# Kernel tuning notes

Hardware: AMD Instinct MI355X
Metric: run time of the kernel (lower is better)

Reference implementation:

```python
import jax, jax.numpy as jnp
import numpy as np

HEAD_DIM = 64
N_HEADS = 12
ROPE_BASE = 10000.0


def _rope_tables(seq_len, head_dim, dtype=jnp.float32):
    half = head_dim // 2
    inv_freq = 1.0 / (ROPE_BASE ** (jnp.arange(0, half, dtype=jnp.float32) / half))
    pos = jnp.arange(seq_len, dtype=jnp.float32)
    freqs = pos[:, None] * inv_freq[None, :]  # (s, half)
    return jnp.cos(freqs).astype(dtype), jnp.sin(freqs).astype(dtype)


def _apply_rope(t, cos, sin):
    # t: (b, h, s, d); rotate-half convention on full head_dim (rope_fraction=1.0)
    d = t.shape[-1]
    t1, t2 = t[..., : d // 2], t[..., d // 2 :]
    cos = cos[None, None, :, :]
    sin = sin[None, None, :, :]
    return jnp.concatenate([t1 * cos - t2 * sin, t1 * sin + t2 * cos], axis=-1)


def setup_inputs() -> dict:
    key = jax.random.key(0)
    ks = jax.random.split(key, 6)
    b, s, d_model = 16, 512, 768
    x = jax.random.normal(ks[0], (b, s, d_model), dtype=jnp.float32)
    chain_ids = jax.random.randint(ks[1], (b, s), 0, 2, dtype=jnp.int32)
    attention_mask = jnp.ones((b, s), dtype=bool)
    inner = N_HEADS * HEAD_DIM
    scale = 0.02
    Wq = jax.random.normal(ks[2], (d_model, inner), dtype=jnp.float32) * scale
    Wk = jax.random.normal(ks[3], (d_model, inner), dtype=jnp.float32) * scale
    Wv = jax.random.normal(ks[4], (d_model, inner), dtype=jnp.float32) * scale
    Wo = jax.random.normal(ks[5], (inner, d_model), dtype=jnp.float32) * scale
    return {"x": x, "chain_ids": chain_ids, "attention_mask": attention_mask,
            "Wq": Wq, "Wk": Wk, "Wv": Wv, "Wo": Wo}


def reference(x, chain_ids, attention_mask, Wq, Wk, Wv, Wo):
    b, s, _ = x.shape
    h, d = N_HEADS, HEAD_DIM
    scale = d ** (-0.5)

    def proj(W):
        return jnp.einsum('bse,ef->bsf', x, W).reshape(b, s, h, d).transpose(0, 2, 1, 3)

    q = proj(Wq)  # (b, h, s, d)
    k = proj(Wk)
    v = proj(Wv)

    cos, sin = _rope_tables(s, d, x.dtype)
    q_rope = _apply_rope(q, cos, sin)
    k_rope = _apply_rope(k, cos, sin)

    scores_intra = jnp.einsum('bhsd,bhtd->bhst', q_rope, k_rope) * scale
    scores_inter = jnp.einsum('bhsd,bhtd->bhst', q, k) * scale

    # intra-chain mask (b, 1, s, s)
    intra = (chain_ids[:, None, :, None] == chain_ids[:, None, None, :])
    merged = jnp.where(intra, scores_intra, scores_inter)

    # additive padding mask (b, 1, 1, s)
    pad = jnp.where(attention_mask[:, None, None, :], 0.0, -jnp.inf).astype(x.dtype)
    merged = merged + pad

    attn = jax.nn.softmax(merged, axis=-1)
    attn = jnp.nan_to_num(attn, nan=0.0)

    out = jnp.einsum('bhst,bhtd->bhsd', attn, v)
    out = out.transpose(0, 2, 1, 3).reshape(b, s, h * d)
    return jnp.einsum('bsf,fe->bse', out, Wo)
```

## Files before the change

kernel.cpp:

```cpp
#include <hip/hip_runtime.h>
#include <stdint.h>
#include <math.h>

#define NB 16
#define NS 512
#define NH 12
#define ND 64
#define NE 768
#define NF 768

typedef __attribute__((ext_vector_type(4))) float  f32x4;
typedef __attribute__((ext_vector_type(8))) short  bf16x8;

#define AS1(p) ((const __attribute__((address_space(1))) unsigned int*)(p))
#define AS3(p) ((__attribute__((address_space(3))) unsigned int*)(p))

__device__ __forceinline__ short f2bf(float f) {
    unsigned u = __builtin_bit_cast(unsigned, f);
    u += 0x7FFFu + ((u >> 16) & 1u);
    return (short)(u >> 16);
}
__device__ __forceinline__ float bf2f(short s) {
    unsigned u = ((unsigned)(unsigned short)s) << 16;
    return __builtin_bit_cast(float, u);
}
__device__ __forceinline__ unsigned pkbf2(float a, float b) {
    return (unsigned)(unsigned short)f2bf(a) | ((unsigned)(unsigned short)f2bf(b) << 16);
}

#define MFMA16(a, b, c) __builtin_amdgcn_mfma_f32_16x16x32_bf16((a), (b), (c), 0, 0, 0)

__device__ __forceinline__ bf16x8 lds_rd8(const short* base, int row, int cb) {
    return *(const bf16x8*)((const char*)base + (((row) * 128 + (cb)) ^ (((row) & 7) << 4)));
}

__global__ __launch_bounds__(256) void prep_all_kernel(
    const float* __restrict__ x, short* __restrict__ xb,
    const float* __restrict__ Wq, const float* __restrict__ Wk,
    const float* __restrict__ Wv, const float* __restrict__ Wo,
    short* __restrict__ Wqt, short* __restrict__ Wkt,
    short* __restrict__ Wvt, short* __restrict__ Wot,
    float* __restrict__ cos_t, float* __restrict__ sin_t,
    const unsigned char* __restrict__ m, int* __restrict__ flag) {
    const int bid = blockIdx.x;
    if (bid < 64) {
        int i = bid * 256 + threadIdx.x;
        int p = i >> 5, j = i & 31;
        float inv_freq = powf(10000.0f, -(float)j / 32.0f);
        float ang = (float)p * inv_freq;
        cos_t[i] = cosf(ang);
        sin_t[i] = sinf(ang);
        return;
    }
    if (bid == 64) {
        __shared__ int any;
        if (threadIdx.x == 0) any = 0;
        __syncthreads();
        int acc = 0;
        for (int i = threadIdx.x; i < NB * NS; i += 256)
            if ((i & 3) && m[i]) acc = 1;
        if (acc) atomicOr(&any, 1);
        __syncthreads();
        if (threadIdx.x == 0) *flag = any;
        return;
    }
    if (bid < 641) {
        int idx = bid - 65;
        int zz = idx / 144, r2 = idx % 144;
        const float* W  = (zz == 0) ? Wq  : (zz == 1) ? Wk  : (zz == 2) ? Wv  : Wo;
        short*       Wt = (zz == 0) ? Wqt : (zz == 1) ? Wkt : (zz == 2) ? Wvt : Wot;
        const int k0 = (r2 / 12) * 64, n0 = (r2 % 12) * 64;
        __shared__ float t[64][65];
        for (int u = threadIdx.x; u < 4096; u += 256) {
            int r = u >> 6, c = u & 63;
            t[r][c] = W[(size_t)(k0 + r) * 768 + n0 + c];
        }
        __syncthreads();
        for (int u = threadIdx.x; u < 4096; u += 256) {
            int c = u >> 6, r = u & 63;
            Wt[(size_t)(n0 + c) * 768 + k0 + r] = f2bf(t[r][c]);
        }
        return;
    }
    int i = ((bid - 641) * 256 + threadIdx.x) * 8;
    float4 a = *(const float4*)&x[i];
    float4 b = *(const float4*)&x[i + 4];
    bf16x8 r = { f2bf(a.x), f2bf(a.y), f2bf(a.z), f2bf(a.w),
                 f2bf(b.x), f2bf(b.y), f2bf(b.z), f2bf(b.w) };
    *(bf16x8*)&xb[i] = r;
}

__global__ __launch_bounds__(256) void gemm_qkv_kernel(const short* __restrict__ xb,
    const short* __restrict__ Wqt, const short* __restrict__ Wkt, const short* __restrict__ Wvt,
    const float* __restrict__ cos_t, const float* __restrict__ sin_t,
    short* __restrict__ qo, short* __restrict__ ko, short* __restrict__ kpo,
    short* __restrict__ vto) {
    const int id = blockIdx.x;
    const int xcd = id & 7, rest = id >> 3;
    const int mq = rest / 18;
    const int nz = rest % 18;
    const int z  = nz / 6;
    const int n0 = (nz % 6) * 128;
    const int m0 = (xcd * 8 + mq) * 128;
    const short* Bt = (z == 0) ? Wqt : (z == 1) ? Wkt : Wvt;
    short*       O  = (z == 0) ? qo  : (z == 1) ? ko  : vto;
    __shared__ short As[2][128 * 64], Bs[2][128 * 64];
    const int tid = threadIdx.x, lane = tid & 63, wave = tid >> 6;
    const int g = lane >> 4, l15 = lane & 15;
    const int wm = wave >> 1, wn = wave & 1;
    f32x4 acc[4][4];
    #pragma unroll
    for (int i = 0; i < 4; ++i)
        #pragma unroll
        for (int j = 0; j < 4; ++j) acc[i][j] = (f32x4){0.f, 0.f, 0.f, 0.f};

    auto STAGE = [&](short* Ad, short* Bd, int kt) {
        const char* Asrc = (const char*)(xb + (size_t)m0 * 768 + kt * 64);
        const char* Bsrc = (const char*)(Bt + (size_t)n0 * 768 + kt * 64);
        #pragma unroll
        for (int p = 0; p < 4; ++p) {
            int dstoff = (wave * 4 + p) * 1024;
            int off = dstoff + lane * 16;
            int row = off >> 7, slot = off & 127;
            int srcs = slot ^ ((row & 7) << 4);
            __builtin_amdgcn_global_load_lds(AS1(Asrc + (size_t)row * 1536 + srcs),
                                             AS3((char*)Ad + dstoff), 16, 0, 0);
            __builtin_amdgcn_global_load_lds(AS1(Bsrc + (size_t)row * 1536 + srcs),
                                             AS3((char*)Bd + dstoff), 16, 0, 0);
        }
    };
    auto COMPUTE = [&](const short* Asb, const short* Bsb) {
        __builtin_amdgcn_s_setprio(1);
        #pragma unroll
        for (int h2 = 0; h2 < 2; ++h2) {
            bf16x8 af[4], bfr[4];
            const int cb = h2 * 64 + g * 16;
            #pragma unroll
            for (int i = 0; i < 4; ++i) {
                af[i]  = lds_rd8(Asb, wm * 64 + i * 16 + l15, cb);
                bfr[i] = lds_rd8(Bsb, wn * 64 + i * 16 + l15, cb);
            }
            #pragma unroll
            for (int i = 0; i < 4; ++i)
                #pragma unroll
                for (int j = 0; j < 4; ++j)
                    acc[i][j] = MFMA16(af[i], bfr[j], acc[i][j]);
        }
        __builtin_amdgcn_s_setprio(0);
    };

    STAGE(As[0], Bs[0], 0);
    asm volatile("s_waitcnt vmcnt(0)" ::: "memory");
    __builtin_amdgcn_s_barrier();
    int cur = 0;
    for (int kt = 0; kt < 11; ++kt) {
        STAGE(As[cur ^ 1], Bs[cur ^ 1], kt + 1);
        COMPUTE(As[cur], Bs[cur]);
        asm volatile("s_waitcnt vmcnt(0)" ::: "memory");
        __builtin_amdgcn_s_barrier();
        cur ^= 1;
    }
    COMPUTE(As[cur], Bs[cur]);

    const int hh = (n0 + wn * 64) >> 6;
    #pragma unroll
    for (int i = 0; i < 4; ++i)
        #pragma unroll
        for (int r = 0; r < 4; ++r) {
            int mm = m0 + wm * 64 + i * 16 + g * 4 + r;
            int bb = mm >> 9, ss = mm & 511;
            if (z == 2) {
                #pragma unroll
                for (int j = 0; j < 4; ++j) {
                    int dd = j * 16 + l15;
                    O[(((size_t)bb * NH + hh) * ND + dd) * NS + ss] = f2bf(acc[i][j][r]);
                }
            } else {
                size_t base = (((size_t)bb * NH + hh) * NS + ss) * ND;
                #pragma unroll
                for (int j = 0; j < 4; ++j)
                    O[base + j * 16 + l15] = f2bf(acc[i][j][r]);
                if (z == 1) {
                    #pragma unroll
                    for (int p2 = 0; p2 < 2; ++p2) {
                        int jf = p2 * 16 + l15;
                        float c = cos_t[ss * 32 + jf], s = sin_t[ss * 32 + jf];
                        float t1 = acc[i][p2][r], t2 = acc[i][p2 + 2][r];
                        kpo[base + jf]      = f2bf(t1 * c - t2 * s);
                        kpo[base + 32 + jf] = f2bf(t1 * s + t2 * c);
                    }
                }
            }
        }
}

__global__ __launch_bounds__(256) void attn_fused_kernel(
    const short* __restrict__ qr, const short* __restrict__ kr, const short* __restrict__ kp,
    const short* __restrict__ vt,
    const float* __restrict__ cos_t, const float* __restrict__ sin_t,
    const int* __restrict__ chain, const void* __restrict__ amask,
    const int* __restrict__ mflag, short* __restrict__ aout) {
    const int lid = blockIdx.x;
    const int xcd = lid & 7, idx = lid >> 3;
    const int qt = idx & 7, bhl = idx >> 3;
    const int bh = xcd * 24 + bhl;
    const int b = bh / 12, h = bh - (bh / 12) * 12;
    const int q0 = qt * 64;

    __shared__ short Kr_s[4096];
    __shared__ short Kp_s[4096];
    __shared__ short Vt_s[4096];
    __shared__ short P_s[4096];
    __shared__ int   ck_a[512];
    __shared__ float kb_a[512];

    const int tid = threadIdx.x, lane = tid & 63, wave = tid >> 6;
    const int g = lane >> 4, l15 = lane & 15;
    const int m_u8 = *mflag;
    const size_t bhNS = (size_t)bh * NS;
    const float SC = 0.18033688011f;

    for (int u = tid; u < NS; u += 256) {
        int gidx = b * NS + u;
        ck_a[u] = chain[gidx];
        int ok = m_u8 ? (int)((const unsigned char*)amask)[gidx] : ((const int*)amask)[gidx];
        kb_a[u] = ok ? 0.f : -INFINITY;
    }
    const char* qrsC = (const char*)(qr + (bhNS + q0) * ND);
    #pragma unroll
    for (int p = 0; p < 2; ++p) {
        int dstoff = (wave * 2 + p) * 1024;
        int off = dstoff + lane * 16;
        int row = off >> 7, slot = off & 127;
        int srcs = slot ^ ((row & 7) << 4);
        __builtin_amdgcn_global_load_lds(AS1(qrsC + (size_t)row * 128 + srcs),
                                         AS3((char*)Kr_s + dstoff), 16, 0, 0);
    }
    __syncthreads();
    const int qrow = wave * 16 + l15;
    bf16x8 fqr0 = lds_rd8(Kr_s, qrow, g * 16);
    bf16x8 fqr1 = lds_rd8(Kr_s, qrow, 64 + g * 16);
    bf16x8 fqp0, fqp1;
    {
        int pos = q0 + qrow;
        float4 c0 = *(const float4*)&cos_t[pos * 32 + g * 8];
        float4 c1 = *(const float4*)&cos_t[pos * 32 + g * 8 + 4];
        float4 s0 = *(const float4*)&sin_t[pos * 32 + g * 8];
        float4 s1 = *(const float4*)&sin_t[pos * 32 + g * 8 + 4];
        float cc[8] = {c0.x, c0.y, c0.z, c0.w, c1.x, c1.y, c1.z, c1.w};
        float ss[8] = {s0.x, s0.y, s0.z, s0.w, s1.x, s1.y, s1.z, s1.w};
        #pragma unroll
        for (int j = 0; j < 8; ++j) {
            float t1 = bf2f(fqr0[j]), t2 = bf2f(fqr1[j]);
            fqp0[j] = f2bf(t1 * cc[j] - t2 * ss[j]);
            fqp1[j] = f2bf(t1 * ss[j] + t2 * cc[j]);
        }
    }
    const int cqv = ck_a[q0 + qrow];

    float m_run = -INFINITY, l_run = 0.f;
    f32x4 accO[4];
    #pragma unroll
    for (int t = 0; t < 4; ++t) accO[t] = (f32x4){0.f, 0.f, 0.f, 0.f};

    const char* krC = (const char*)(kr + bhNS * ND);
    const char* kpC = (const char*)(kp + bhNS * ND);
    const char* vtC = (const char*)(vt + bhNS * ND);

    for (int kv = 0; kv < 8; ++kv) {
        const int k0s = kv * 64;
        __syncthreads();
        #pragma unroll
        for (int p = 0; p < 2; ++p) {
            int dstoff = (wave * 2 + p) * 1024;
            int off = dstoff + lane * 16;
            int row = off >> 7, slot = off & 127;
            int srcs = slot ^ ((row & 7) << 4);
            size_t koff = (size_t)(k0s + row) * 128 + srcs;
            __builtin_amdgcn_global_load_lds(AS1(krC + koff), AS3((char*)Kr_s + dstoff), 16, 0, 0);
            __builtin_amdgcn_global_load_lds(AS1(kpC + koff), AS3((char*)Kp_s + dstoff), 16, 0, 0);
            __builtin_amdgcn_global_load_lds(AS1(vtC + (size_t)row * 1024 + k0s * 2 + srcs),
                                             AS3((char*)Vt_s + dstoff), 16, 0, 0);
        }
        __syncthreads();

        float pm[4][4];
        float tm = -INFINITY;
        __builtin_amdgcn_s_setprio(1);
        #pragma unroll
        for (int t = 0; t < 4; ++t) {
            bf16x8 akr0 = lds_rd8(Kr_s, t * 16 + l15, g * 16);
            bf16x8 akr1 = lds_rd8(Kr_s, t * 16 + l15, 64 + g * 16);
            bf16x8 akp0 = lds_rd8(Kp_s, t * 16 + l15, g * 16);
            bf16x8 akp1 = lds_rd8(Kp_s, t * 16 + l15, 64 + g * 16);
            f32x4 sr = (f32x4){0.f, 0.f, 0.f, 0.f};
            f32x4 sp = (f32x4){0.f, 0.f, 0.f, 0.f};
            sr = MFMA16(akr0, fqr0, sr);
            sr = MFMA16(akr1, fqr1, sr);
            sp = MFMA16(akp0, fqp0, sp);
            sp = MFMA16(akp1, fqp1, sp);
            int4   ck4 = *(const int4*)&ck_a[k0s + t * 16 + g * 4];
            float4 kb4 = *(const float4*)&kb_a[k0s + t * 16 + g * 4];
            const int   ckk[4] = {ck4.x, ck4.y, ck4.z, ck4.w};
            const float kbb[4] = {kb4.x, kb4.y, kb4.z, kb4.w};
            #pragma unroll
            for (int r = 0; r < 4; ++r) {
                float sv = (cqv == ckk[r]) ? sp[r] : sr[r];
                sv = sv * SC + kbb[r];
                pm[t][r] = sv;
                tm = fmaxf(tm, sv);
            }
        }
        __builtin_amdgcn_s_setprio(0);

        tm = fmaxf(tm, __shfl_xor(tm, 16));
        tm = fmaxf(tm, __shfl_xor(tm, 32));
        bool skip = __all(tm - m_run <= 8.f);
        float mnew, fac;
        if (skip) { mnew = m_run; fac = 1.f; }
        else      { mnew = fmaxf(m_run, tm); fac = exp2f(m_run - mnew); }
        float psum = 0.f;
        if (mnew == -INFINITY) {
            #pragma unroll
            for (int t = 0; t < 4; ++t)
                #pragma unroll
                for (int r = 0; r < 4; ++r) pm[t][r] = 0.f;
            fac = 1.f;
        } else {
            #pragma unroll
            for (int t = 0; t < 4; ++t)
                #pragma unroll
                for (int r = 0; r < 4; ++r) {
                    float p = exp2f(pm[t][r] - mnew);
                    pm[t][r] = p;
                    psum += p;
                }
        }
        psum += __shfl_xor(psum, 16);
        psum += __shfl_xor(psum, 32);
        l_run = l_run * fac + psum;
        m_run = mnew;

        char* pwave = (char*)P_s + wave * 2048;
        int psw = (l15 & 7) << 4;
        #pragma unroll
        for (int t = 0; t < 4; ++t) {
            unsigned u0 = pkbf2(pm[t][0], pm[t][1]);
            unsigned u1 = pkbf2(pm[t][2], pm[t][3]);
            uint2 pk = {u0, u1};
            *(uint2*)(pwave + ((l15 * 128 + t * 32 + g * 8) ^ psw)) = pk;
        }
        if (!skip) {
            float f4[4];
            #pragma unroll
            for (int r = 0; r < 4; ++r) f4[r] = __shfl(fac, g * 4 + r);
            #pragma unroll
            for (int t = 0; t < 4; ++t) {
                f32x4 a = accO[t];
                a[0] *= f4[0]; a[1] *= f4[1]; a[2] *= f4[2]; a[3] *= f4[3];
                accO[t] = a;
            }
        }
        bf16x8 pa0 = *(const bf16x8*)(pwave + ((l15 * 128 + g * 16) ^ psw));
        bf16x8 pa1 = *(const bf16x8*)(pwave + ((l15 * 128 + 64 + g * 16) ^ psw));
        __builtin_amdgcn_s_setprio(1);
        #pragma unroll
        for (int dt = 0; dt < 4; ++dt) {
            bf16x8 vb0 = lds_rd8(Vt_s, dt * 16 + l15, g * 16);
            bf16x8 vb1 = lds_rd8(Vt_s, dt * 16 + l15, 64 + g * 16);
            accO[dt] = MFMA16(pa0, vb0, accO[dt]);
            accO[dt] = MFMA16(pa1, vb1, accO[dt]);
        }
        __builtin_amdgcn_s_setprio(0);
    }

    float inv[4];
    #pragma unroll
    for (int r = 0; r < 4; ++r) {
        float lv = __shfl(l_run, g * 4 + r);
        inv[r] = (lv > 0.f) ? 1.f / lv : 0.f;
    }
    #pragma unroll
    for (int dt = 0; dt < 4; ++dt)
        #pragma unroll
        for (int r = 0; r < 4; ++r) {
            int row = b * NS + q0 + wave * 16 + g * 4 + r;
            aout[(size_t)row * NF + h * ND + dt * 16 + l15] = f2bf(accO[dt][r] * inv[r]);
        }
}

__global__ __launch_bounds__(256) void gemm_out_kernel(const short* __restrict__ A,
    const short* __restrict__ Wot, float* __restrict__ out) {
    const int id = blockIdx.x;
    const int xcd = id & 7, rest = id >> 3;
    const int mq = rest / 6;
    const int n0 = (rest % 6) * 128;
    const int m0 = (xcd * 16 + mq) * 64;
    __shared__ short As[2][64 * 64], Bs[2][128 * 64];
    const int tid = threadIdx.x, lane = tid & 63, wave = tid >> 6;
    const int g = lane >> 4, l15 = lane & 15;
    const int wm = wave >> 1, wn = wave & 1;
    f32x4 acc[2][4];
    #pragma unroll
    for (int i = 0; i < 2; ++i)
        #pragma unroll
        for (int j = 0; j < 4; ++j) acc[i][j] = (f32x4){0.f, 0.f, 0.f, 0.f};

    auto STAGE = [&](short* Ad, short* Bd, int kt) {
        const char* Asrc = (const char*)(A   + (size_t)m0 * 768 + kt * 64);
        const char* Bsrc = (const char*)(Wot + (size_t)n0 * 768 + kt * 64);
        #pragma unroll
        for (int p = 0; p < 2; ++p) {
            int dstoff = (wave * 2 + p) * 1024;
            int off = dstoff + lane * 16;
            int row = off >> 7, slot = off & 127;
            int srcs = slot ^ ((row & 7) << 4);
            __builtin_amdgcn_global_load_lds(AS1(Asrc + (size_t)row * 1536 + srcs),
                                             AS3((char*)Ad + dstoff), 16, 0, 0);
        }
        #pragma unroll
        for (int p = 0; p < 4; ++p) {
            int dstoff = (wave * 4 + p) * 1024;
            int off = dstoff + lane * 16;
            int row = off >> 7, slot = off & 127;
            int srcs = slot ^ ((row & 7) << 4);
            __builtin_amdgcn_global_load_lds(AS1(Bsrc + (size_t)row * 1536 + srcs),
                                             AS3((char*)Bd + dstoff), 16, 0, 0);
        }
    };
    auto COMPUTE = [&](const short* Asb, const short* Bsb) {
        __builtin_amdgcn_s_setprio(1);
        #pragma unroll
        for (int h2 = 0; h2 < 2; ++h2) {
            bf16x8 af[2], bfr[4];
            const int cb = h2 * 64 + g * 16;
            #pragma unroll
            for (int i = 0; i < 2; ++i)
                af[i]  = lds_rd8(Asb, wm * 32 + i * 16 + l15, cb);
            #pragma unroll
            for (int j = 0; j < 4; ++j)
                bfr[j] = lds_rd8(Bsb, wn * 64 + j * 16 + l15, cb);
            #pragma unroll
            for (int i = 0; i < 2; ++i)
                #pragma unroll
                for (int j = 0; j < 4; ++j)
                    acc[i][j] = MFMA16(af[i], bfr[j], acc[i][j]);
        }
        __builtin_amdgcn_s_setprio(0);
    };

    STAGE(As[0], Bs[0], 0);
    asm volatile("s_waitcnt vmcnt(0)" ::: "memory");
    __builtin_amdgcn_s_barrier();
    int cur = 0;
    for (int kt = 0; kt < 11; ++kt) {
        STAGE(As[cur ^ 1], Bs[cur ^ 1], kt + 1);
        COMPUTE(As[cur], Bs[cur]);
        asm volatile("s_waitcnt vmcnt(0)" ::: "memory");
        __builtin_amdgcn_s_barrier();
        cur ^= 1;
    }
    COMPUTE(As[cur], Bs[cur]);

    #pragma unroll
    for (int i = 0; i < 2; ++i)
        #pragma unroll
        for (int r = 0; r < 4; ++r) {
            int mm = m0 + wm * 32 + i * 16 + g * 4 + r;
            #pragma unroll
            for (int j = 0; j < 4; ++j) {
                int n = n0 + wn * 64 + j * 16 + l15;
                out[(size_t)mm * NE + n] = acc[i][j][r];
            }
        }
}

extern "C" void kernel_launch(void* const* d_in, const int* in_sizes, int n_in,
                              void* d_out, int out_size, void* d_ws, size_t ws_size,
                              hipStream_t stream) {
    const float* x     = (const float*)d_in[0];
    const int*   chain = (const int*)d_in[1];
    const void*  amask = d_in[2];
    const float* Wq = (const float*)d_in[3];
    const float* Wk = (const float*)d_in[4];
    const float* Wv = (const float*)d_in[5];
    const float* Wo = (const float*)d_in[6];
    float* out = (float*)d_out;

    const size_t QSZ = (size_t)NB * NH * NS * ND;
    char* w = (char*)d_ws;
    float* cos_t = (float*)w;  w += (size_t)NS * 32 * 4;
    float* sin_t = (float*)w;  w += (size_t)NS * 32 * 4;
    int*   mflag = (int*)w;    w += 256;
    short* xb    = (short*)w;  w += (size_t)8192 * 768 * 2;
    short* Wqt   = (short*)w;  w += (size_t)768 * 768 * 2;
    short* Wkt   = (short*)w;  w += (size_t)768 * 768 * 2;
    short* Wvt   = (short*)w;  w += (size_t)768 * 768 * 2;
    short* Wot   = (short*)w;  w += (size_t)768 * 768 * 2;
    short* q_raw = (short*)w;  w += QSZ * 2;
    short* k_raw = (short*)w;  w += QSZ * 2;
    short* k_rop = (short*)w;  w += QSZ * 2;
    short* vtr   = (short*)w;  w += QSZ * 2;
    short* aout  = xb;

    prep_all_kernel<<<dim3(3713), dim3(256), 0, stream>>>(x, xb, Wq, Wk, Wv, Wo,
                                                          Wqt, Wkt, Wvt, Wot,
                                                          cos_t, sin_t,
                                                          (const unsigned char*)amask, mflag);
    gemm_qkv_kernel<<<dim3(1152), dim3(256), 0, stream>>>(xb, Wqt, Wkt, Wvt, cos_t, sin_t,
                                                          q_raw, k_raw, k_rop, vtr);
    attn_fused_kernel<<<dim3(1536), dim3(256), 0, stream>>>(q_raw, k_raw, k_rop, vtr,
                                                            cos_t, sin_t, chain, amask, mflag, aout);
    gemm_out_kernel<<<dim3(768), dim3(256), 0, stream>>>(aout, Wot, out);
}
```

Before: 152.2 us.

## Halve QKV GEMM M-tile and register-prefetch K/V tiles in attention

The QKV projection GEMM now uses 64-row M tiles instead of 128, doubling the grid to 2304 blocks for better occupancy and load balance at the cost of less B-tile reuse. The attention kernel replaces direct global-to-LDS loads with register prefetch: the next K/K-rope/V tile is loaded into registers while the current tile is computed, then written to LDS at the top of the next iteration. This hides global load latency behind compute, adds an extra barrier per iteration and raises register pressure.

```diff
diff --git a/kernel.cpp b/kernel.cpp
--- a/kernel.cpp
+++ b/kernel.cpp
@@ -101,30 +101,37 @@
     const int nz = rest % 18;
     const int z  = nz / 6;
     const int n0 = (nz % 6) * 128;
-    const int m0 = (xcd * 8 + mq) * 128;
+    const int m0 = (xcd * 16 + mq) * 64;
     const short* Bt = (z == 0) ? Wqt : (z == 1) ? Wkt : Wvt;
     short*       O  = (z == 0) ? qo  : (z == 1) ? ko  : vto;
-    __shared__ short As[2][128 * 64], Bs[2][128 * 64];
+    __shared__ short As[2][64 * 64], Bs[2][128 * 64];
     const int tid = threadIdx.x, lane = tid & 63, wave = tid >> 6;
     const int g = lane >> 4, l15 = lane & 15;
     const int wm = wave >> 1, wn = wave & 1;
-    f32x4 acc[4][4];
-    #pragma unroll
-    for (int i = 0; i < 4; ++i)
+    f32x4 acc[2][4];
+    #pragma unroll
+    for (int i = 0; i < 2; ++i)
         #pragma unroll
         for (int j = 0; j < 4; ++j) acc[i][j] = (f32x4){0.f, 0.f, 0.f, 0.f};
 
     auto STAGE = [&](short* Ad, short* Bd, int kt) {
         const char* Asrc = (const char*)(xb + (size_t)m0 * 768 + kt * 64);
         const char* Bsrc = (const char*)(Bt + (size_t)n0 * 768 + kt * 64);
+        #pragma unroll
+        for (int p = 0; p < 2; ++p) {
+            int dstoff = (wave * 2 + p) * 1024;
+            int off = dstoff + lane * 16;
+            int row = off >> 7, slot = off & 127;
+            int srcs = slot ^ ((row & 7) << 4);
+            __builtin_amdgcn_global_load_lds(AS1(Asrc + (size_t)row * 1536 + srcs),
+                                             AS3((char*)Ad + dstoff), 16, 0, 0);
+        }
         #pragma unroll
         for (int p = 0; p < 4; ++p) {
             int dstoff = (wave * 4 + p) * 1024;
             int off = dstoff + lane * 16;
             int row = off >> 7, slot = off & 127;
             int srcs = slot ^ ((row & 7) << 4);
-            __builtin_amdgcn_global_load_lds(AS1(Asrc + (size_t)row * 1536 + srcs),
-                                             AS3((char*)Ad + dstoff), 16, 0, 0);
             __builtin_amdgcn_global_load_lds(AS1(Bsrc + (size_t)row * 1536 + srcs),
                                              AS3((char*)Bd + dstoff), 16, 0, 0);
         }
@@ -133,15 +140,16 @@
         __builtin_amdgcn_s_setprio(1);
         #pragma unroll
         for (int h2 = 0; h2 < 2; ++h2) {
-            bf16x8 af[4], bfr[4];
+            bf16x8 af[2], bfr[4];
             const int cb = h2 * 64 + g * 16;
             #pragma unroll
-            for (int i = 0; i < 4; ++i) {
-                af[i]  = lds_rd8(Asb, wm * 64 + i * 16 + l15, cb);
-                bfr[i] = lds_rd8(Bsb, wn * 64 + i * 16 + l15, cb);
-            }
-            #pragma unroll
-            for (int i = 0; i < 4; ++i)
+            for (int i = 0; i < 2; ++i)
+                af[i]  = lds_rd8(Asb, wm * 32 + i * 16 + l15, cb);
+            #pragma unroll
+            for (int j = 0; j < 4; ++j)
+                bfr[j] = lds_rd8(Bsb, wn * 64 + j * 16 + l15, cb);
+            #pragma unroll
+            for (int i = 0; i < 2; ++i)
                 #pragma unroll
                 for (int j = 0; j < 4; ++j)
                     acc[i][j] = MFMA16(af[i], bfr[j], acc[i][j]);
@@ -164,10 +172,10 @@
 
     const int hh = (n0 + wn * 64) >> 6;
     #pragma unroll
-    for (int i = 0; i < 4; ++i)
+    for (int i = 0; i < 2; ++i)
         #pragma unroll
         for (int r = 0; r < 4; ++r) {
-            int mm = m0 + wm * 64 + i * 16 + g * 4 + r;
+            int mm = m0 + wm * 32 + i * 16 + g * 4 + r;
             int bb = mm >> 9, ss = mm & 511;
             if (z == 2) {
                 #pragma unroll
@@ -267,22 +275,41 @@
     const char* kpC = (const char*)(kp + bhNS * ND);
     const char* vtC = (const char*)(vt + bhNS * ND);
 
+    int off_[2], row_[2], srcs_[2];
+    #pragma unroll
+    for (int p = 0; p < 2; ++p) {
+        int dstoff = (wave * 2 + p) * 1024;
+        off_[p]  = dstoff + lane * 16;
+        row_[p]  = off_[p] >> 7;
+        srcs_[p] = (off_[p] & 127) ^ ((row_[p] & 7) << 4);
+    }
+    uint4 rK0, rK1, rP0, rP1, rV0, rV1;
+    auto LOADREGS = [&](int kv) {
+        const int k0s = kv * 64;
+        rK0 = *(const uint4*)(krC + (size_t)(k0s + row_[0]) * 128 + srcs_[0]);
+        rK1 = *(const uint4*)(krC + (size_t)(k0s + row_[1]) * 128 + srcs_[1]);
+        rP0 = *(const uint4*)(kpC + (size_t)(k0s + row_[0]) * 128 + srcs_[0]);
+        rP1 = *(const uint4*)(kpC + (size_t)(k0s + row_[1]) * 128 + srcs_[1]);
+        rV0 = *(const uint4*)(vtC + (size_t)row_[0] * 1024 + (size_t)k0s * 2 + srcs_[0]);
+        rV1 = *(const uint4*)(vtC + (size_t)row_[1] * 1024 + (size_t)k0s * 2 + srcs_[1]);
+    };
+    auto WRITELDS = [&]() {
+        *(uint4*)((char*)Kr_s + off_[0]) = rK0;
+        *(uint4*)((char*)Kr_s + off_[1]) = rK1;
+        *(uint4*)((char*)Kp_s + off_[0]) = rP0;
+        *(uint4*)((char*)Kp_s + off_[1]) = rP1;
+        *(uint4*)((char*)Vt_s + off_[0]) = rV0;
+        *(uint4*)((char*)Vt_s + off_[1]) = rV1;
+    };
+
+    LOADREGS(0);
+    __syncthreads();
+
     for (int kv = 0; kv < 8; ++kv) {
         const int k0s = kv * 64;
+        WRITELDS();
         __syncthreads();
-        #pragma unroll
-        for (int p = 0; p < 2; ++p) {
-            int dstoff = (wave * 2 + p) * 1024;
-            int off = dstoff + lane * 16;
-            int row = off >> 7, slot = off & 127;
-            int srcs = slot ^ ((row & 7) << 4);
-            size_t koff = (size_t)(k0s + row) * 128 + srcs;
-            __builtin_amdgcn_global_load_lds(AS1(krC + koff), AS3((char*)Kr_s + dstoff), 16, 0, 0);
-            __builtin_amdgcn_global_load_lds(AS1(kpC + koff), AS3((char*)Kp_s + dstoff), 16, 0, 0);
-            __builtin_amdgcn_global_load_lds(AS1(vtC + (size_t)row * 1024 + k0s * 2 + srcs),
-                                             AS3((char*)Vt_s + dstoff), 16, 0, 0);
-        }
-        __syncthreads();
+        if (kv < 7) LOADREGS(kv + 1);
 
         float pm[4][4];
         float tm = -INFINITY;
@@ -372,6 +399,7 @@
             accO[dt] = MFMA16(pa1, vb1, accO[dt]);
         }
         __builtin_amdgcn_s_setprio(0);
+        __syncthreads();
     }
 
     float inv[4];
@@ -507,7 +535,7 @@
                                                           Wqt, Wkt, Wvt, Wot,
                                                           cos_t, sin_t,
                                                           (const unsigned char*)amask, mflag);
-    gemm_qkv_kernel<<<dim3(1152), dim3(256), 0, stream>>>(xb, Wqt, Wkt, Wvt, cos_t, sin_t,
+    gemm_qkv_kernel<<<dim3(2304), dim3(256), 0, stream>>>(xb, Wqt, Wkt, Wvt, cos_t, sin_t,
                                                           q_raw, k_raw, k_rop, vtr);
     attn_fused_kernel<<<dim3(1536), dim3(256), 0, stream>>>(q_raw, k_raw, k_rop, vtr,
                                                             cos_t, sin_t, chain, amask, mflag, aout);
```

Result: faster. 143.3 us (-5.8%).
